# Kernel optimization log

Hardware: AMD Instinct MI355X
Metric: run time of the kernel (lower is better)

Reference implementation:

```python
import jax, jax.numpy as jnp
import numpy as np

DIM = 256
HID = DIM * 16

def setup_inputs() -> dict:
    key = jax.random.key(0)
    ks = jax.random.split(key, 6)
    B, L = 4, 2048
    x = jax.random.normal(ks[0], (B, L, DIM), dtype=jnp.float32)
    # nn.Linear(dim, hidden): weight [H, D], bias [H]
    WB = jax.random.normal(ks[1], (HID, DIM), dtype=jnp.float32) / np.sqrt(DIM)
    bB = jax.random.normal(ks[2], (HID,), dtype=jnp.float32) * 0.01
    # nn.Linear(hidden, dim): weight [D, H], bias [D]
    WC = jax.random.normal(ks[3], (DIM, HID), dtype=jnp.float32) / np.sqrt(HID)
    bC = jax.random.normal(ks[4], (DIM,), dtype=jnp.float32) * 0.01
    A = jax.random.normal(ks[5], (HID,), dtype=jnp.float32)
    return {"x": x, "WB": WB, "bB": bB, "WC": WC, "bC": bC, "A": A}

def reference(x, WB, bB, WC, bC, A):
    # b = B(x): [B, L, H]
    b = jnp.einsum('bld,hd->blh', x, WB) + bB
    a = jax.nn.sigmoid(A)  # [H], time-invariant decay
    # h_t = a * h_{t-1} + b_t  (h_0 from zero state) -> associative scan over L
    a_seq = jnp.broadcast_to(a, b.shape)
    def comb(c1, c2):
        a1, u1 = c1
        a2, u2 = c2
        return (a1 * a2, a2 * u1 + u2)
    _, h = jax.lax.associative_scan(comb, (a_seq, b), axis=1)  # [B, L, H]
    # C(h): [B, L, D]
    return jnp.einsum('blh,dh->bld', h, WC) + bC
```

## Files before the change

kernel.cpp:

```cpp
#include <hip/hip_runtime.h>
#include <hip/hip_bf16.h>

#define DIMSZ 256
#define HID 4096
#define BATCH 4
#define SEQ 2048
#define NCH 64
#define CLEN 32
#define SPLITK2 4
#define KCHUNK (HID / SPLITK2)
#define BM2 64

typedef __bf16 bf16_t;
typedef __bf16 bf16x8 __attribute__((ext_vector_type(8)));
typedef float  f32x4  __attribute__((ext_vector_type(4)));

__device__ __forceinline__ float sigmoidf_dev(float x) {
    return 1.0f / (1.0f + __expf(-x));
}

__device__ __forceinline__ void load_lds16(const bf16_t* g, bf16_t* l) {
    __builtin_amdgcn_global_load_lds(
        (const __attribute__((address_space(1))) void*)g,
        (__attribute__((address_space(3))) void*)l,
        16, 0, 0);
}

__device__ __forceinline__ bf16x8 cvt8(const float* p) {
    bf16x8 o;
    #pragma unroll
    for (int j = 0; j < 8; j++) o[j] = (bf16_t)p[j];
    return o;
}

__global__ void prep_kernel(const float* __restrict__ x,
                            const float* __restrict__ WB,
                            const float* __restrict__ WC,
                            bf16_t* __restrict__ xt,
                            bf16_t* __restrict__ WBt,
                            bf16_t* __restrict__ Wt) {
    int i = blockIdx.x * blockDim.x + threadIdx.x;
    if (i < 262144) {
        int lane = i & 63, m16 = (i >> 6) & 511, ks = i >> 15;
        int row = m16 * 16 + (lane & 15);
        int k   = ks * 32 + (lane >> 4) * 8;
        *(bf16x8*)&xt[(size_t)i * 8] = cvt8(&x[(size_t)row * DIMSZ + k]);
    } else if (i < 393216) {
        int j = i - 262144;
        int lane = j & 63, n16 = (j >> 6) & 255, ks = j >> 14;
        int row = n16 * 16 + (lane & 15);
        int k   = ks * 32 + (lane >> 4) * 8;
        *(bf16x8*)&WBt[(size_t)j * 8] = cvt8(&WB[(size_t)row * DIMSZ + k]);
    } else {
        int j = i - 393216;
        int lane = j & 63, g = (j >> 6) & 15, ks = j >> 10;
        int row = g * 16 + (lane & 15);
        int k   = ks * 32 + (lane >> 4) * 8;
        *(bf16x8*)&Wt[(size_t)j * 8] = cvt8(&WC[(size_t)row * HID + k]);
    }
}

__global__ __launch_bounds__(256)
void gemm1_fused(const bf16_t* __restrict__ xt, const bf16_t* __restrict__ WBt,
                 const float* __restrict__ bias, const float* __restrict__ Adecay,
                 bf16_t* __restrict__ Cg, float* __restrict__ totals)
{
    constexpr int N = HID;
    constexpr int LDTILE = 136;
    __shared__ bf16_t tile[128 * LDTILE];

    const int tid = threadIdx.x, wave = tid >> 6, lane = tid & 63;
    const int wm = wave >> 1, wn = wave & 1, q = lane >> 4, r16 = lane & 15;
    const int mBase = blockIdx.x * 128, nBase = blockIdx.y * 128;
    const int m16Base = blockIdx.x * 8 + wm * 4;
    const int n16Base = blockIdx.y * 8 + wn * 4;

    f32x4 acc[4][4] = {};

    #pragma unroll 2
    for (int ks = 0; ks < 8; ks++) {
        bf16x8 af[4], bfr[4];
        #pragma unroll
        for (int mt = 0; mt < 4; mt++)
            af[mt] = *(const bf16x8*)&xt[(((size_t)ks * 512 + m16Base + mt) * 64 + lane) * 8];
        #pragma unroll
        for (int nt = 0; nt < 4; nt++)
            bfr[nt] = *(const bf16x8*)&WBt[(((size_t)ks * 256 + n16Base + nt) * 64 + lane) * 8];
        #pragma unroll
        for (int mt = 0; mt < 4; mt++)
            #pragma unroll
            for (int nt = 0; nt < 4; nt++)
                acc[mt][nt] = __builtin_amdgcn_mfma_f32_16x16x32_bf16(
                    af[mt], bfr[nt], acc[mt][nt], 0, 0, 0);
    }

    #pragma unroll
    for (int nt = 0; nt < 4; nt++) {
        const int chl = wn * 64 + nt * 16 + r16;
        const float bv = bias[nBase + chl];
        #pragma unroll
        for (int mt = 0; mt < 4; mt++) {
            const int t0 = wm * 64 + mt * 16 + q * 4;
            #pragma unroll
            for (int rg = 0; rg < 4; rg++)
                tile[(t0 + rg) * LDTILE + chl] = (bf16_t)(acc[mt][nt][rg] + bv);
        }
    }
    __syncthreads();

    #pragma unroll
    for (int p = 0; p < 8; p++) {
        const int t = p * 16 + (tid >> 4);
        const int ch8 = (tid & 15) << 3;
        *(bf16x8*)&Cg[(size_t)(mBase + t) * N + nBase + ch8] =
            *(const bf16x8*)&tile[t * LDTILE + ch8];
    }

    #pragma unroll
    for (int t = 0; t < 2; t++) {
        int task = tid + t * 256;
        int ch = task & 127, ck = task >> 7;
        float a = sigmoidf_dev(Adecay[nBase + ch]);
        float tot = 0.f;
        #pragma unroll 8
        for (int i = 0; i < CLEN; i++)
            tot = a * tot + (float)tile[(ck * CLEN + i) * LDTILE + ch];
        int batch = mBase >> 11;
        int cg = ((mBase & 2047) >> 5) + ck;
        totals[(size_t)(batch * NCH + cg) * HID + nBase + ch] = tot;
    }
}

__global__ void scan_carries_kernel(const float* __restrict__ totals,
                                    const float* __restrict__ Adecay,
                                    float* __restrict__ carries)
{
    int gid = blockIdx.x * 64 + threadIdx.x;
    int ch    = gid & (HID - 1);
    int batch = gid >> 12;
    float a = sigmoidf_dev(Adecay[ch]);
    float aC = a;
    #pragma unroll
    for (int i = 0; i < 5; i++) aC *= aC;
    float carry = 0.f;
    #pragma unroll 8
    for (int c = 0; c < NCH; c++) {
        size_t idx = (size_t)(batch * NCH + c) * HID + ch;
        carries[idx] = carry;
        carry = aC * carry + totals[idx];
    }
}

__global__ __launch_bounds__(256)
void gemm2_fused(const bf16_t* __restrict__ bv, const bf16_t* __restrict__ Wt,
                 const float* __restrict__ Adecay, const float* __restrict__ carries,
                 float* __restrict__ P)
{
    constexpr int N = DIMSZ;
    constexpr int CKSTRIDE = BM2 * 32 + 32;
    __shared__ bf16_t hs[8 * CKSTRIDE];

    const int tid = threadIdx.x, wave = tid >> 6, lane = tid & 63;
    const int q = lane >> 4, r16 = lane & 15;
    const int mBase = blockIdx.x * BM2;
    const int kBase = blockIdx.y * KCHUNK;
    const int batch = mBase >> 11;
    const int chunk0 = (mBase & 2047) >> 5;

    f32x4 acc[4][4] = {};

    for (int s = 0; s < KCHUNK / 256; s++) {
        const int chSlab = kBase + s * 256;

        if (s > 0) __syncthreads();

        #pragma unroll
        for (int i = 0; i < 8; i++) {
            int ck = wave * 2 + (i >> 2);
            int g  = i & 3;
            load_lds16(&bv[(size_t)(mBase + g * 16 + (lane >> 2)) * HID
                           + chSlab + ck * 32 + ((lane & 3) << 3)],
                       &hs[ck * CKSTRIDE + g * 512]);
        }
        __syncthreads();

        {
            const int ck = tid >> 5, ch = tid & 31;
            const int c = chSlab + ck * 32 + ch;
            const float a = sigmoidf_dev(Adecay[c]);
            float st = carries[(size_t)(batch * NCH + chunk0) * HID + c];
            bf16_t* hp = &hs[ck * CKSTRIDE + ch];
            #pragma unroll 8
            for (int t = 0; t < BM2; t++) {
                st = a * st + (float)hp[t * 32];
                hp[t * 32] = (bf16_t)st;
            }
        }
        __syncthreads();

        const int ksBase = (kBase >> 5) + s * 8;
        #pragma unroll 2
        for (int ck = 0; ck < 8; ck++) {
            bf16x8 af[4], bfr[4];
            #pragma unroll
            for (int nt = 0; nt < 4; nt++)
                bfr[nt] = *(const bf16x8*)&Wt[
                    (((size_t)(ksBase + ck) * 16 + wave * 4 + nt) * 64 + lane) * 8];
            #pragma unroll
            for (int mt = 0; mt < 4; mt++)
                af[mt] = *(const bf16x8*)&hs[ck * CKSTRIDE + (mt * 16 + r16) * 32 + q * 8];
            #pragma unroll
            for (int mt = 0; mt < 4; mt++)
                #pragma unroll
                for (int nt = 0; nt < 4; nt++)
                    acc[mt][nt] = __builtin_amdgcn_mfma_f32_16x16x32_bf16(
                        af[mt], bfr[nt], acc[mt][nt], 0, 0, 0);
        }
    }

    float* Pb = P + (size_t)blockIdx.y * (BATCH * SEQ) * N;
    #pragma unroll
    for (int nt = 0; nt < 4; nt++) {
        const int col = wave * 64 + nt * 16 + r16;
        #pragma unroll
        for (int mt = 0; mt < 4; mt++) {
            const int row0 = mBase + mt * 16 + q * 4;
            #pragma unroll
            for (int rg = 0; rg < 4; rg++)
                Pb[(size_t)(row0 + rg) * N + col] = acc[mt][nt][rg];
        }
    }
}

__global__ void reduce_out_kernel(const float* __restrict__ P,
                                  const float* __restrict__ bias,
                                  float* __restrict__ out, int MN4) {
    int i = blockIdx.x * blockDim.x + threadIdx.x;
    if (i >= MN4) return;
    int n4 = i & (DIMSZ / 4 - 1);
    float4 acc = ((const float4*)bias)[n4];
    #pragma unroll
    for (int s = 0; s < SPLITK2; s++) {
        float4 p = ((const float4*)P)[(size_t)s * MN4 + i];
        acc.x += p.x; acc.y += p.y; acc.z += p.z; acc.w += p.w;
    }
    ((float4*)out)[i] = acc;
}

extern "C" void kernel_launch(void* const* d_in, const int* in_sizes, int n_in,
                              void* d_out, int out_size, void* d_ws, size_t ws_size,
                              hipStream_t stream)
{
    const float* x  = (const float*)d_in[0];
    const float* WB = (const float*)d_in[1];
    const float* bB = (const float*)d_in[2];
    const float* WC = (const float*)d_in[3];
    const float* bC = (const float*)d_in[4];
    const float* A  = (const float*)d_in[5];

    char* ws = (char*)d_ws;
    size_t off = 0;
    bf16_t* xt   = (bf16_t*)(ws + off); off += (size_t)BATCH * SEQ * DIMSZ * 2;
    bf16_t* WBt  = (bf16_t*)(ws + off); off += (size_t)HID * DIMSZ * 2;
    bf16_t* Wt   = (bf16_t*)(ws + off); off += (size_t)DIMSZ * HID * 2;
    bf16_t* bbuf = (bf16_t*)(ws + off); off += (size_t)BATCH * SEQ * HID * 2;
    float* partials = (float*)(ws + off); off += (size_t)SPLITK2 * BATCH * SEQ * DIMSZ * 4;
    float* totals   = (float*)(ws + off); off += (size_t)BATCH * NCH * HID * 4;
    float* carries  = (float*)(ws + off); off += (size_t)BATCH * NCH * HID * 4;

    const int M = BATCH * SEQ;

    prep_kernel<<<2048, 256, 0, stream>>>(x, WB, WC, xt, WBt, Wt);

    dim3 g1(M / 128, HID / 128);
    gemm1_fused<<<g1, 256, 0, stream>>>(xt, WBt, bB, A, bbuf, totals);

    scan_carries_kernel<<<256, 64, 0, stream>>>(totals, A, carries);

    dim3 g2(M / BM2, SPLITK2);
    gemm2_fused<<<g2, 256, 0, stream>>>(bbuf, Wt, A, carries, partials);
    reduce_out_kernel<<<(M * DIMSZ / 4 + 255) / 256, 256, 0, stream>>>(
        partials, bC, (float*)d_out, M * DIMSZ / 4);
}
```

Baseline: 153.6 us.

## Fuse carry scan into gemm2 and split in-block scan into two chains

Removes the separate carry-scan kernel and its carries buffer. Each gemm2 block now rebuilds its starting carry by scanning the chunk totals up to its own position, overlapping with the async LDS loads. The in-block 64-row scan becomes two independent 32-row chains, the second seeded with the carry after the first chunk, to halve the serial dependency length. The trade is redundant per-block work: up to 63 strided global reads of totals per thread per slab, which grows with the block's position in the sequence.

```diff
diff --git a/kernel.cpp b/kernel.cpp
--- a/kernel.cpp
+++ b/kernel.cpp
@@ -131,29 +131,9 @@
     }
 }
 
-__global__ void scan_carries_kernel(const float* __restrict__ totals,
-                                    const float* __restrict__ Adecay,
-                                    float* __restrict__ carries)
-{
-    int gid = blockIdx.x * 64 + threadIdx.x;
-    int ch    = gid & (HID - 1);
-    int batch = gid >> 12;
-    float a = sigmoidf_dev(Adecay[ch]);
-    float aC = a;
-    #pragma unroll
-    for (int i = 0; i < 5; i++) aC *= aC;
-    float carry = 0.f;
-    #pragma unroll 8
-    for (int c = 0; c < NCH; c++) {
-        size_t idx = (size_t)(batch * NCH + c) * HID + ch;
-        carries[idx] = carry;
-        carry = aC * carry + totals[idx];
-    }
-}
-
 __global__ __launch_bounds__(256)
 void gemm2_fused(const bf16_t* __restrict__ bv, const bf16_t* __restrict__ Wt,
-                 const float* __restrict__ Adecay, const float* __restrict__ carries,
+                 const float* __restrict__ Adecay, const float* __restrict__ totals,
                  float* __restrict__ P)
 {
     constexpr int N = DIMSZ;
@@ -182,33 +162,45 @@
                            + chSlab + ck * 32 + ((lane & 3) << 3)],
                        &hs[ck * CKSTRIDE + g * 512]);
         }
+
+        const int ck = tid >> 5, ch = tid & 31;
+        const int c = chSlab + ck * 32 + ch;
+        const float a = sigmoidf_dev(Adecay[c]);
+        float aC = a;
+        #pragma unroll
+        for (int i = 0; i < 5; i++) aC *= aC;
+        const float* tp = &totals[(size_t)batch * NCH * HID + c];
+        float carry0 = 0.f;
+        for (int cc = 0; cc < chunk0; cc++)
+            carry0 = aC * carry0 + tp[(size_t)cc * HID];
+        const float carry1 = aC * carry0 + tp[(size_t)chunk0 * HID];
+
         __syncthreads();
 
         {
-            const int ck = tid >> 5, ch = tid & 31;
-            const int c = chSlab + ck * 32 + ch;
-            const float a = sigmoidf_dev(Adecay[c]);
-            float st = carries[(size_t)(batch * NCH + chunk0) * HID + c];
             bf16_t* hp = &hs[ck * CKSTRIDE + ch];
+            float st0 = carry0, st1 = carry1;
             #pragma unroll 8
-            for (int t = 0; t < BM2; t++) {
-                st = a * st + (float)hp[t * 32];
-                hp[t * 32] = (bf16_t)st;
+            for (int t = 0; t < 32; t++) {
+                st0 = a * st0 + (float)hp[t * 32];
+                st1 = a * st1 + (float)hp[(t + 32) * 32];
+                hp[t * 32]        = (bf16_t)st0;
+                hp[(t + 32) * 32] = (bf16_t)st1;
             }
         }
         __syncthreads();
 
         const int ksBase = (kBase >> 5) + s * 8;
         #pragma unroll 2
-        for (int ck = 0; ck < 8; ck++) {
+        for (int cki = 0; cki < 8; cki++) {
             bf16x8 af[4], bfr[4];
             #pragma unroll
             for (int nt = 0; nt < 4; nt++)
                 bfr[nt] = *(const bf16x8*)&Wt[
-                    (((size_t)(ksBase + ck) * 16 + wave * 4 + nt) * 64 + lane) * 8];
+                    (((size_t)(ksBase + cki) * 16 + wave * 4 + nt) * 64 + lane) * 8];
             #pragma unroll
             for (int mt = 0; mt < 4; mt++)
-                af[mt] = *(const bf16x8*)&hs[ck * CKSTRIDE + (mt * 16 + r16) * 32 + q * 8];
+                af[mt] = *(const bf16x8*)&hs[cki * CKSTRIDE + (mt * 16 + r16) * 32 + q * 8];
             #pragma unroll
             for (int mt = 0; mt < 4; mt++)
                 #pragma unroll
@@ -266,7 +258,6 @@
     bf16_t* bbuf = (bf16_t*)(ws + off); off += (size_t)BATCH * SEQ * HID * 2;
     float* partials = (float*)(ws + off); off += (size_t)SPLITK2 * BATCH * SEQ * DIMSZ * 4;
     float* totals   = (float*)(ws + off); off += (size_t)BATCH * NCH * HID * 4;
-    float* carries  = (float*)(ws + off); off += (size_t)BATCH * NCH * HID * 4;
 
     const int M = BATCH * SEQ;
 
@@ -275,10 +266,8 @@
     dim3 g1(M / 128, HID / 128);
     gemm1_fused<<<g1, 256, 0, stream>>>(xt, WBt, bB, A, bbuf, totals);
 
-    scan_carries_kernel<<<256, 64, 0, stream>>>(totals, A, carries);
-
     dim3 g2(M / BM2, SPLITK2);
-    gemm2_fused<<<g2, 256, 0, stream>>>(bbuf, Wt, A, carries, partials);
+    gemm2_fused<<<g2, 256, 0, stream>>>(bbuf, Wt, A, totals, partials);
     reduce_out_kernel<<<(M * DIMSZ / 4 + 255) / 256, 256, 0, stream>>>(
         partials, bC, (float*)d_out, M * DIMSZ / 4);
 }
```

Result: slower. 201.9 us (+31.5%).

## Store split-K partials in bf16 via LDS staging and halve gemm2 row tile

Applied to the files above, without the earlier changes.

The split-K partials of the second GEMM are now written as bf16 instead of fp32. They are staged through shared memory so each thread can issue coalesced 16-byte row stores, and the reduce kernel reads them eight at a time. The gemm2 row tile shrinks from 64 to 32, which doubles the block count, and the carry and decay loads are hoisted above the barrier so they overlap the async LDS loads. This targets the global traffic for writing and re-reading the partials, at the cost of bf16 rounding before the split-K sum and twice as many reloads of the weight fragments.

```diff
diff --git a/kernel.cpp b/kernel.cpp
--- a/kernel.cpp
+++ b/kernel.cpp
@@ -9,7 +9,7 @@
 #define CLEN 32
 #define SPLITK2 4
 #define KCHUNK (HID / SPLITK2)
-#define BM2 64
+#define BM2 32
 
 typedef __bf16 bf16_t;
 typedef __bf16 bf16x8 __attribute__((ext_vector_type(8)));
@@ -154,9 +154,8 @@
 __global__ __launch_bounds__(256)
 void gemm2_fused(const bf16_t* __restrict__ bv, const bf16_t* __restrict__ Wt,
                  const float* __restrict__ Adecay, const float* __restrict__ carries,
-                 float* __restrict__ P)
+                 bf16_t* __restrict__ P)
 {
-    constexpr int N = DIMSZ;
     constexpr int CKSTRIDE = BM2 * 32 + 32;
     __shared__ bf16_t hs[8 * CKSTRIDE];
 
@@ -167,7 +166,7 @@
     const int batch = mBase >> 11;
     const int chunk0 = (mBase & 2047) >> 5;
 
-    f32x4 acc[4][4] = {};
+    f32x4 acc[2][4] = {};
 
     for (int s = 0; s < KCHUNK / 256; s++) {
         const int chSlab = kBase + s * 256;
@@ -175,20 +174,22 @@
         if (s > 0) __syncthreads();
 
         #pragma unroll
-        for (int i = 0; i < 8; i++) {
-            int ck = wave * 2 + (i >> 2);
-            int g  = i & 3;
+        for (int i = 0; i < 4; i++) {
+            int ck = wave * 2 + (i >> 1);
+            int g  = i & 1;
             load_lds16(&bv[(size_t)(mBase + g * 16 + (lane >> 2)) * HID
                            + chSlab + ck * 32 + ((lane & 3) << 3)],
                        &hs[ck * CKSTRIDE + g * 512]);
         }
+
+        const int ck = tid >> 5, ch = tid & 31;
+        const int c = chSlab + ck * 32 + ch;
+        const float a = sigmoidf_dev(Adecay[c]);
+        float st = carries[(size_t)(batch * NCH + chunk0) * HID + c];
+
         __syncthreads();
 
         {
-            const int ck = tid >> 5, ch = tid & 31;
-            const int c = chSlab + ck * 32 + ch;
-            const float a = sigmoidf_dev(Adecay[c]);
-            float st = carries[(size_t)(batch * NCH + chunk0) * HID + c];
             bf16_t* hp = &hs[ck * CKSTRIDE + ch];
             #pragma unroll 8
             for (int t = 0; t < BM2; t++) {
@@ -200,17 +201,17 @@
 
         const int ksBase = (kBase >> 5) + s * 8;
         #pragma unroll 2
-        for (int ck = 0; ck < 8; ck++) {
-            bf16x8 af[4], bfr[4];
+        for (int cki = 0; cki < 8; cki++) {
+            bf16x8 af[2], bfr[4];
             #pragma unroll
             for (int nt = 0; nt < 4; nt++)
                 bfr[nt] = *(const bf16x8*)&Wt[
-                    (((size_t)(ksBase + ck) * 16 + wave * 4 + nt) * 64 + lane) * 8];
-            #pragma unroll
-            for (int mt = 0; mt < 4; mt++)
-                af[mt] = *(const bf16x8*)&hs[ck * CKSTRIDE + (mt * 16 + r16) * 32 + q * 8];
-            #pragma unroll
-            for (int mt = 0; mt < 4; mt++)
+                    (((size_t)(ksBase + cki) * 16 + wave * 4 + nt) * 64 + lane) * 8];
+            #pragma unroll
+            for (int mt = 0; mt < 2; mt++)
+                af[mt] = *(const bf16x8*)&hs[cki * CKSTRIDE + (mt * 16 + r16) * 32 + q * 8];
+            #pragma unroll
+            for (int mt = 0; mt < 2; mt++)
                 #pragma unroll
                 for (int nt = 0; nt < 4; nt++)
                     acc[mt][nt] = __builtin_amdgcn_mfma_f32_16x16x32_bf16(
@@ -218,33 +219,47 @@
         }
     }
 
-    float* Pb = P + (size_t)blockIdx.y * (BATCH * SEQ) * N;
+    __syncthreads();
     #pragma unroll
     for (int nt = 0; nt < 4; nt++) {
         const int col = wave * 64 + nt * 16 + r16;
         #pragma unroll
-        for (int mt = 0; mt < 4; mt++) {
-            const int row0 = mBase + mt * 16 + q * 4;
+        for (int mt = 0; mt < 2; mt++)
             #pragma unroll
             for (int rg = 0; rg < 4; rg++)
-                Pb[(size_t)(row0 + rg) * N + col] = acc[mt][nt][rg];
-        }
-    }
-}
-
-__global__ void reduce_out_kernel(const float* __restrict__ P,
+                hs[(mt * 16 + q * 4 + rg) * 264 + col] = (bf16_t)acc[mt][nt][rg];
+    }
+    __syncthreads();
+
+    bf16_t* Pb = P + (size_t)blockIdx.y * (BATCH * SEQ) * DIMSZ;
+    #pragma unroll
+    for (int p = 0; p < 4; p++) {
+        int task = p * 256 + tid;
+        int r = task >> 5, g8 = (task & 31) << 3;
+        *(bf16x8*)&Pb[(size_t)(mBase + r) * DIMSZ + g8] =
+            *(const bf16x8*)&hs[r * 264 + g8];
+    }
+}
+
+__global__ void reduce_out_kernel(const bf16_t* __restrict__ P,
                                   const float* __restrict__ bias,
-                                  float* __restrict__ out, int MN4) {
+                                  float* __restrict__ out, int nTask) {
     int i = blockIdx.x * blockDim.x + threadIdx.x;
-    if (i >= MN4) return;
-    int n4 = i & (DIMSZ / 4 - 1);
-    float4 acc = ((const float4*)bias)[n4];
-    #pragma unroll
-    for (int s = 0; s < SPLITK2; s++) {
-        float4 p = ((const float4*)P)[(size_t)s * MN4 + i];
-        acc.x += p.x; acc.y += p.y; acc.z += p.z; acc.w += p.w;
-    }
-    ((float4*)out)[i] = acc;
+    if (i >= nTask) return;
+    int n8 = (i & 31) << 3;
+    size_t off = (size_t)i * 8;
+    float v[8];
+    #pragma unroll
+    for (int j = 0; j < 8; j++) v[j] = bias[n8 + j];
+    #pragma unroll
+    for (int sp = 0; sp < SPLITK2; sp++) {
+        bf16x8 p = *(const bf16x8*)&P[(size_t)sp * (BATCH * SEQ) * DIMSZ + off];
+        #pragma unroll
+        for (int j = 0; j < 8; j++) v[j] += (float)p[j];
+    }
+    float4* o4 = (float4*)&out[off];
+    o4[0] = make_float4(v[0], v[1], v[2], v[3]);
+    o4[1] = make_float4(v[4], v[5], v[6], v[7]);
 }
 
 extern "C" void kernel_launch(void* const* d_in, const int* in_sizes, int n_in,
@@ -264,7 +279,7 @@
     bf16_t* WBt  = (bf16_t*)(ws + off); off += (size_t)HID * DIMSZ * 2;
     bf16_t* Wt   = (bf16_t*)(ws + off); off += (size_t)DIMSZ * HID * 2;
     bf16_t* bbuf = (bf16_t*)(ws + off); off += (size_t)BATCH * SEQ * HID * 2;
-    float* partials = (float*)(ws + off); off += (size_t)SPLITK2 * BATCH * SEQ * DIMSZ * 4;
+    bf16_t* partials = (bf16_t*)(ws + off); off += (size_t)SPLITK2 * BATCH * SEQ * DIMSZ * 2;
     float* totals   = (float*)(ws + off); off += (size_t)BATCH * NCH * HID * 4;
     float* carries  = (float*)(ws + off); off += (size_t)BATCH * NCH * HID * 4;
 
@@ -279,6 +294,8 @@
 
     dim3 g2(M / BM2, SPLITK2);
     gemm2_fused<<<g2, 256, 0, stream>>>(bbuf, Wt, A, carries, partials);
-    reduce_out_kernel<<<(M * DIMSZ / 4 + 255) / 256, 256, 0, stream>>>(
-        partials, bC, (float*)d_out, M * DIMSZ / 4);
-}
+
+    int nTask = M * DIMSZ / 8;
+    reduce_out_kernel<<<(nTask + 255) / 256, 256, 0, stream>>>(
+        partials, bC, (float*)d_out, nTask);
+}
```

New measurement: 149.9 us. -2.4%, faster.
